# Kernel tuning notes

Hardware: AMD Instinct MI355X
Metric: run time of the kernel (lower is better)

Reference implementation:

```python
import jax, jax.numpy as jnp
import numpy as np

N = 4096          # nodes == num_rels (forced by einsum 'ij,ijk->ik')
IN_F = 128
OUT_F = 128


def setup_inputs() -> dict:
    key = jax.random.key(0)
    k1, k2, k3, k4 = jax.random.split(key, 4)
    xavier = float(np.sqrt(2.0 / (IN_F + OUT_F)))
    return {
        "input": jax.random.normal(k1, (N, IN_F), dtype=jnp.float32),
        "adjacency_matrix": jax.random.uniform(k2, (N, N), dtype=jnp.float32),
        "rel_matrix": jax.random.normal(k3, (N, OUT_F, OUT_F), dtype=jnp.float32) * xavier,
        "weights": jax.random.normal(k4, (N, IN_F, OUT_F), dtype=jnp.float32) * xavier,
        "bias": jnp.zeros((OUT_F,), dtype=jnp.float32),
    }


def reference(input, adjacency_matrix, rel_matrix, weights, bias):
    # per-node transform: support[n, k] = sum_j input[n, j] * weights[n, j, k]
    support = jnp.einsum('nj,njk->nk', input, weights)          # [N, out]
    # per-node relational combine: out[n, j] = sum_k rel_matrix[n, j, k] * support[n, k]
    out = jnp.einsum('njk,nk->nj', rel_matrix, support)         # [N, out]
    # dense adjacency aggregation + bias
    out = jnp.matmul(adjacency_matrix, out) + bias              # [N, out]
    return out
```

## Files before the change

kernel.cpp:

```cpp
#include <hip/hip_runtime.h>
#include <hip/hip_bf16.h>

typedef __attribute__((ext_vector_type(4))) float floatx4;
typedef __bf16 bf16x8 __attribute__((ext_vector_type(8)));

static __device__ __forceinline__ unsigned short f2bf(float x) {
    union { float f; unsigned int u; } v; v.f = x;
    unsigned int u = v.u;
    unsigned int r = u + 0x7FFF + ((u >> 16) & 1);
    return (unsigned short)(r >> 16);
}

__global__ __launch_bounds__(256) void node_transform(
    const float* __restrict__ input,
    const float* __restrict__ rel,
    const float* __restrict__ wts,
    unsigned int* __restrict__ h_t)
{
    __shared__ float s_in[2][128];
    __shared__ float s_part[2][4][128];
    __shared__ float s_sup[2][128];
    __shared__ float s_h[2][128];

    const int tid = threadIdx.x;
    const int b = blockIdx.x;

    if (tid < 64) {
        float4 v = ((const float4*)input)[b * 64 + tid];
        ((float4*)&s_in[0][0])[tid] = v;
    }
    __syncthreads();

    const int node = tid >> 7;
    const int tl   = tid & 127;
    const int n    = b * 2 + node;

    {
        const int jg = tl >> 5;
        const int kq = tl & 31;
        const float4* W4 = (const float4*)(wts + (size_t)n * 16384);
        float4 acc = {0.f, 0.f, 0.f, 0.f};
        const int j0 = jg * 32;
        #pragma unroll 8
        for (int jj = 0; jj < 32; ++jj) {
            const int j = j0 + jj;
            const float x = s_in[node][j];
            const float4 w = W4[j * 32 + kq];
            acc.x += x * w.x; acc.y += x * w.y;
            acc.z += x * w.z; acc.w += x * w.w;
        }
        ((float4*)&s_part[node][jg][0])[kq] = acc;
    }
    __syncthreads();
    s_sup[node][tl] = s_part[node][0][tl] + s_part[node][1][tl]
                    + s_part[node][2][tl] + s_part[node][3][tl];
    __syncthreads();

    {
        const int wnode = tl >> 6;
        const int lane  = tl & 63;
        const int half  = lane >> 5;
        const int l     = lane & 31;
        const float4* R4 = (const float4*)(rel + (size_t)n * 16384);
        const float4 sv = ((const float4*)&s_sup[node][0])[l];
        #pragma unroll 4
        for (int it = 0; it < 32; ++it) {
            const int j = wnode * 64 + it * 2 + half;
            const float4 r = R4[j * 32 + l];
            float p = r.x * sv.x + r.y * sv.y + r.z * sv.z + r.w * sv.w;
            p += __shfl_xor(p, 1);
            p += __shfl_xor(p, 2);
            p += __shfl_xor(p, 4);
            p += __shfl_xor(p, 8);
            p += __shfl_xor(p, 16);
            if (l == 0) s_h[node][j] = p;
        }
    }
    __syncthreads();

    if (tid < 128) {
        const unsigned int lo = f2bf(s_h[0][tid]);
        const unsigned int hi = f2bf(s_h[1][tid]);
        h_t[tid * 2048 + b] = lo | (hi << 16);
    }
}

__global__ __launch_bounds__(512) void agg_gemm(
    const float* __restrict__ A,
    const unsigned short* __restrict__ ht,
    const float* __restrict__ bias,
    float* __restrict__ out)
{
    __shared__ __align__(16) unsigned short As[16][136];
    __shared__ __align__(16) unsigned short Bs[128][136];

    const int tid  = threadIdx.x;
    const int wave = tid >> 6;
    const int lane = tid & 63;
    const int m0   = blockIdx.x * 16;

    floatx4 acc = {0.f, 0.f, 0.f, 0.f};

    const int ar = tid >> 5;
    const int ac = (tid & 31) * 4;
    const int bj = tid >> 2;
    const int bs = tid & 3;

    for (int kb = 0; kb < 4096; kb += 128) {
        __syncthreads();
        {
            const float4 v = *(const float4*)(A + (size_t)(m0 + ar) * 4096 + kb + ac);
            const unsigned int p0 = (unsigned int)f2bf(v.x) | ((unsigned int)f2bf(v.y) << 16);
            const unsigned int p1 = (unsigned int)f2bf(v.z) | ((unsigned int)f2bf(v.w) << 16);
            *(uint2*)&As[ar][ac] = make_uint2(p0, p1);
        }
        {
            const unsigned short* src = ht + (size_t)bj * 4096 + kb + bs * 8;
            #pragma unroll
            for (int i = 0; i < 4; ++i) {
                const uint4 v = *(const uint4*)(src + i * 32);
                *(uint4*)&Bs[bj][bs * 8 + i * 32] = v;
            }
        }
        __syncthreads();
        const int mn = lane & 15;
        const int kq = lane >> 4;
        const unsigned short* arow = &As[mn][kq * 8];
        const unsigned short* brow = &Bs[wave * 16 + mn][kq * 8];
        #pragma unroll
        for (int k0 = 0; k0 < 128; k0 += 32) {
            const bf16x8 af = *(const bf16x8*)(arow + k0);
            const bf16x8 bfr = *(const bf16x8*)(brow + k0);
            acc = __builtin_amdgcn_mfma_f32_16x16x32_bf16(af, bfr, acc, 0, 0, 0);
        }
    }

    const int col = wave * 16 + (lane & 15);
    const int r0  = (lane >> 4) * 4;
    const float bv = bias[col];
    #pragma unroll
    for (int r = 0; r < 4; ++r) {
        out[(size_t)(m0 + r0 + r) * 128 + col] = acc[r] + bv;
    }
}

extern "C" void kernel_launch(void* const* d_in, const int* in_sizes, int n_in,
                              void* d_out, int out_size, void* d_ws, size_t ws_size,
                              hipStream_t stream) {
    const float* input = (const float*)d_in[0];
    const float* adj   = (const float*)d_in[1];
    const float* rel   = (const float*)d_in[2];
    const float* wts   = (const float*)d_in[3];
    const float* bias  = (const float*)d_in[4];
    float* out = (float*)d_out;

    unsigned int* h_t = (unsigned int*)d_ws;

    node_transform<<<2048, 256, 0, stream>>>(input, rel, wts, h_t);
    agg_gemm<<<256, 512, 0, stream>>>(adj, (const unsigned short*)d_ws, bias, out);
}
```

Before: 572.0 us.

## Load MFMA operands directly from global memory, dropping LDS staging and barriers

```diff
diff --git a/kernel.cpp b/kernel.cpp
--- a/kernel.cpp
+++ b/kernel.cpp
@@ -9,6 +9,13 @@
     unsigned int u = v.u;
     unsigned int r = u + 0x7FFF + ((u >> 16) & 1);
     return (unsigned short)(r >> 16);
+}
+
+static __device__ __forceinline__ __bf16 tobf(float f) {
+    __hip_bfloat16 h = __float2bfloat16(f);
+    __bf16 r;
+    __builtin_memcpy(&r, &h, 2);
+    return r;
 }
 
 __global__ __launch_bounds__(256) void node_transform(
@@ -91,52 +98,33 @@
     const float* __restrict__ bias,
     float* __restrict__ out)
 {
-    __shared__ __align__(16) unsigned short As[16][136];
-    __shared__ __align__(16) unsigned short Bs[128][136];
-
     const int tid  = threadIdx.x;
     const int wave = tid >> 6;
     const int lane = tid & 63;
     const int m0   = blockIdx.x * 16;
+    const int mn   = lane & 15;
+    const int kq   = lane >> 4;
+
+    const float*          arow = A  + (size_t)(m0 + mn) * 4096 + kq * 8;
+    const unsigned short* brow = ht + (size_t)(wave * 16 + mn) * 4096 + kq * 8;
 
     floatx4 acc = {0.f, 0.f, 0.f, 0.f};
 
-    const int ar = tid >> 5;
-    const int ac = (tid & 31) * 4;
-    const int bj = tid >> 2;
-    const int bs = tid & 3;
-
-    for (int kb = 0; kb < 4096; kb += 128) {
-        __syncthreads();
-        {
-            const float4 v = *(const float4*)(A + (size_t)(m0 + ar) * 4096 + kb + ac);
-            const unsigned int p0 = (unsigned int)f2bf(v.x) | ((unsigned int)f2bf(v.y) << 16);
-            const unsigned int p1 = (unsigned int)f2bf(v.z) | ((unsigned int)f2bf(v.w) << 16);
-            *(uint2*)&As[ar][ac] = make_uint2(p0, p1);
-        }
-        {
-            const unsigned short* src = ht + (size_t)bj * 4096 + kb + bs * 8;
-            #pragma unroll
-            for (int i = 0; i < 4; ++i) {
-                const uint4 v = *(const uint4*)(src + i * 32);
-                *(uint4*)&Bs[bj][bs * 8 + i * 32] = v;
-            }
-        }
-        __syncthreads();
-        const int mn = lane & 15;
-        const int kq = lane >> 4;
-        const unsigned short* arow = &As[mn][kq * 8];
-        const unsigned short* brow = &Bs[wave * 16 + mn][kq * 8];
-        #pragma unroll
-        for (int k0 = 0; k0 < 128; k0 += 32) {
-            const bf16x8 af = *(const bf16x8*)(arow + k0);
-            const bf16x8 bfr = *(const bf16x8*)(brow + k0);
-            acc = __builtin_amdgcn_mfma_f32_16x16x32_bf16(af, bfr, acc, 0, 0, 0);
-        }
+    #pragma unroll 4
+    for (int kb = 0; kb < 4096; kb += 32) {
+        const float4 a0 = *(const float4*)(arow + kb);
+        const float4 a1 = *(const float4*)(arow + kb + 4);
+        const bf16x8 bfr = *(const bf16x8*)(brow + kb);
+        bf16x8 af;
+        af[0] = tobf(a0.x); af[1] = tobf(a0.y);
+        af[2] = tobf(a0.z); af[3] = tobf(a0.w);
+        af[4] = tobf(a1.x); af[5] = tobf(a1.y);
+        af[6] = tobf(a1.z); af[7] = tobf(a1.w);
+        acc = __builtin_amdgcn_mfma_f32_16x16x32_bf16(af, bfr, acc, 0, 0, 0);
     }
 
-    const int col = wave * 16 + (lane & 15);
-    const int r0  = (lane >> 4) * 4;
+    const int col = wave * 16 + mn;
+    const int r0  = kq * 4;
     const float bv = bias[col];
     #pragma unroll
     for (int r = 0; r < 4; ++r) {
```

Measured after the change: 616.6 us. +7.8%, slower.

## Split aggregation GEMM along K into four partials with separate reduce-bias kernel

Applied to the files above, without the earlier changes.

```diff
diff --git a/kernel.cpp b/kernel.cpp
--- a/kernel.cpp
+++ b/kernel.cpp
@@ -85,11 +85,10 @@
     }
 }
 
-__global__ __launch_bounds__(512) void agg_gemm(
+__global__ __launch_bounds__(512) void agg_gemm_splitk(
     const float* __restrict__ A,
     const unsigned short* __restrict__ ht,
-    const float* __restrict__ bias,
-    float* __restrict__ out)
+    float* __restrict__ part)
 {
     __shared__ __align__(16) unsigned short As[16][136];
     __shared__ __align__(16) unsigned short Bs[128][136];
@@ -97,7 +96,9 @@
     const int tid  = threadIdx.x;
     const int wave = tid >> 6;
     const int lane = tid & 63;
-    const int m0   = blockIdx.x * 16;
+    const int s    = blockIdx.x & 3;
+    const int m0   = (blockIdx.x >> 2) * 16;
+    const int kbase = s * 1024;
 
     floatx4 acc = {0.f, 0.f, 0.f, 0.f};
 
@@ -106,7 +107,7 @@
     const int bj = tid >> 2;
     const int bs = tid & 3;
 
-    for (int kb = 0; kb < 4096; kb += 128) {
+    for (int kb = kbase; kb < kbase + 1024; kb += 128) {
         __syncthreads();
         {
             const float4 v = *(const float4*)(A + (size_t)(m0 + ar) * 4096 + kb + ac);
@@ -129,7 +130,7 @@
         const unsigned short* brow = &Bs[wave * 16 + mn][kq * 8];
         #pragma unroll
         for (int k0 = 0; k0 < 128; k0 += 32) {
-            const bf16x8 af = *(const bf16x8*)(arow + k0);
+            const bf16x8 af  = *(const bf16x8*)(arow + k0);
             const bf16x8 bfr = *(const bf16x8*)(brow + k0);
             acc = __builtin_amdgcn_mfma_f32_16x16x32_bf16(af, bfr, acc, 0, 0, 0);
         }
@@ -137,11 +138,31 @@
 
     const int col = wave * 16 + (lane & 15);
     const int r0  = (lane >> 4) * 4;
-    const float bv = bias[col];
+    float* dst = part + ((size_t)s * 4096 + m0 + r0) * 128 + col;
     #pragma unroll
     for (int r = 0; r < 4; ++r) {
-        out[(size_t)(m0 + r0 + r) * 128 + col] = acc[r] + bv;
+        dst[(size_t)r * 128] = acc[r];
     }
+}
+
+__global__ __launch_bounds__(256) void reduce_bias(
+    const float* __restrict__ part,
+    const float* __restrict__ bias,
+    float* __restrict__ out)
+{
+    const int f = blockIdx.x * 256 + threadIdx.x;
+    const float4* p4 = (const float4*)part;
+    const float4 b = ((const float4*)bias)[f & 31];
+    float4 s0 = p4[f];
+    float4 s1 = p4[131072 + f];
+    float4 s2 = p4[262144 + f];
+    float4 s3 = p4[393216 + f];
+    float4 r;
+    r.x = s0.x + s1.x + s2.x + s3.x + b.x;
+    r.y = s0.y + s1.y + s2.y + s3.y + b.y;
+    r.z = s0.z + s1.z + s2.z + s3.z + b.z;
+    r.w = s0.w + s1.w + s2.w + s3.w + b.w;
+    ((float4*)out)[f] = r;
 }
 
 extern "C" void kernel_launch(void* const* d_in, const int* in_sizes, int n_in,
@@ -155,7 +176,9 @@
     float* out = (float*)d_out;
 
     unsigned int* h_t = (unsigned int*)d_ws;
+    float* part = (float*)((char*)d_ws + (1 << 20));
 
     node_transform<<<2048, 256, 0, stream>>>(input, rel, wts, h_t);
-    agg_gemm<<<256, 512, 0, stream>>>(adj, (const unsigned short*)d_ws, bias, out);
+    agg_gemm_splitk<<<1024, 512, 0, stream>>>(adj, (const unsigned short*)d_ws, part);
+    reduce_bias<<<512, 256, 0, stream>>>(part, bias, out);
 }
```

Result: no change. 562.3 us (-1.7%).
